# Kernel tuning notes

Measured on AMD Instinct MI355X. Metric: run time of the kernel, lower is better.

Reference implementation:

```python
import jax, jax.numpy as jnp
import numpy as np

BETA = 1.0
POWER_ITERS = 9
EPS = 1e-12  # F.normalize default eps


def _normalize(v):
    # L2 normalize over dim=1 of [B, N, 1], matching F.normalize(x, dim=1)
    n = jnp.linalg.norm(v, axis=1, keepdims=True)
    return v / jnp.maximum(n, EPS)


def _dominant_eigenvalue(A, x):
    # A: [B, N, N], x: [B, N, 1]
    for _ in range(POWER_ITERS):
        x = _normalize(jnp.matmul(A, x))
    Ax = jnp.matmul(A, x)[..., 0]              # [B, N]
    num = jnp.sum(Ax * x[..., 0], axis=1)      # x^T A x
    den = jnp.sum(x[..., 0] ** 2, axis=1)      # ||x||^2 (== 1 after normalize)
    return num / den, x


def setup_inputs() -> dict:
    key = jax.random.key(0)
    k1, k2 = jax.random.split(key)
    B, C, H, W = 256, 2048, 7, 7
    x = jax.random.normal(k1, (B, C, H, W), dtype=jnp.float32)
    x0 = _normalize(jax.random.normal(k2, (B, H * W, 1), dtype=jnp.float32))
    return {"x": x, "x0": x0}


def reference(x, x0):
    B, C, H, W = x.shape
    N = H * W
    Wm = x.reshape(B, C, N)
    # ATA = W^T W : [B, N, N]
    ATA = jnp.einsum('bcn,bcm->bnm', Wm, Wm)
    # first power iteration: largest eigenvalue; x0 is a no_grad constant
    largest, x1 = _dominant_eigenvalue(ATA, jax.lax.stop_gradient(x0))
    I = jnp.eye(N, dtype=ATA.dtype)
    shifted = ATA - largest[:, None, None] * I
    # second power iteration warm-started from detached x1 (torch stores last_x detached)
    tmp, _ = _dominant_eigenvalue(shifted, jax.lax.stop_gradient(x1))
    smallest = tmp + largest
    penalty = BETA * (largest / smallest - 1.0) ** 2
    return jnp.sum(penalty) / B
```

## Files before the change

### kernel.cpp

```cpp
#include <hip/hip_runtime.h>
#include <hip/hip_bf16.h>
#include <stdint.h>


#define BATCH 256
#define CDIM  2048
#define NDIM  49
#define GROUPS 2
#define GK    (CDIM / GROUPS)
#define CHUNK 64
#define NCHUNK (GK / CHUNK)
#define ITEMS (NDIM * (CHUNK / 8))
#define CHUNK_FLOATS (CHUNK * NDIM)

typedef __bf16 bf16x8 __attribute__((ext_vector_type(8)));
typedef float  f32x16 __attribute__((ext_vector_type(16)));
typedef float  f32x4  __attribute__((ext_vector_type(4)));

union V16 {
  f32x4  f4;
  bf16x8 b8;
};

__device__ __forceinline__ void load8(const float* __restrict__ g,
                                      float (&r)[8]) {
#pragma unroll
  for (int j = 0; j < 8; ++j) r[j] = g[j * NDIM];
}

__device__ __forceinline__ void cvt_store(const float (&r)[8], float* Hb,
                                          float* Lb, int w) {
  bf16x8 hv, lv;
#pragma unroll
  for (int j = 0; j < 8; ++j) {
    float e = r[j];
    __bf16 h = (__bf16)e;
    hv[j] = h;
    lv[j] = (__bf16)(e - (float)h);
  }
  V16 a, b;
  a.b8 = hv;
  b.b8 = lv;
  *(f32x4*)(Hb + w) = a.f4;
  *(f32x4*)(Lb + w) = b.f4;
}

__device__ __forceinline__ void comp16(const float* Hb, const float* Lb,
                                       int m, int n, int hf, f32x16& c1,
                                       f32x16& c2, f32x16& c3) {
  const f32x4* H = (const f32x4*)Hb;
  const f32x4* L = (const f32x4*)Lb;
#pragma unroll
  for (int s = 0; s < 4; ++s) {
    const int blk = 2 * s + hf;
    V16 ah, al, bh, bl;
    ah.f4 = H[m * 8 + (blk ^ (m & 7))];
    al.f4 = L[m * 8 + (blk ^ (m & 7))];
    bh.f4 = H[n * 8 + (blk ^ (n & 7))];
    bl.f4 = L[n * 8 + (blk ^ (n & 7))];
    c1 = __builtin_amdgcn_mfma_f32_32x32x16_bf16(ah.b8, bh.b8, c1, 0, 0, 0);
    c2 = __builtin_amdgcn_mfma_f32_32x32x16_bf16(ah.b8, bl.b8, c2, 0, 0, 0);
    c3 = __builtin_amdgcn_mfma_f32_32x32x16_bf16(al.b8, bh.b8, c3, 0, 0, 0);
  }
}

__global__ __launch_bounds__(512) void fused_kernel(
    const float* __restrict__ x, const float* __restrict__ x0,
    float* __restrict__ pen) {
  __shared__ __align__(16) float lds[GROUPS * 8192];
  __shared__ __align__(16) float A[NDIM * NDIM + 3];

  const int tid  = threadIdx.x;
  const int b    = blockIdx.x;
  const int g    = tid >> 8;
  const int ltid = tid & 255;
  const int lane = tid & 63;
  const int gw   = (tid >> 6) & 3;
  const int ln   = lane & 31;
  const int hf   = lane >> 5;
  const int qm = gw >> 1, qn = gw & 1;
  const int m = qm * 32 + ln;
  const int n = qn * 32 + ln;

  float* const buf0 = lds + g * 8192;
  float* const buf1 = lds + g * 8192 + 4096;

  const float* gbase = x + (size_t)b * (CDIM * NDIM)
                         + (size_t)g * (GK * NDIM);

  const int i0 = ltid;
  const int i1 = ltid + 256;
  const bool v1 = (i1 < ITEMS);
  const int kq0 = (i0 * 1338) >> 16;
  const int n0  = i0 - 49 * kq0;
  const int kq1 = (i1 * 1338) >> 16;
  const int n1  = i1 - 49 * kq1;
  const int g0  = kq0 * (8 * NDIM) + n0;
  const int g1  = kq1 * (8 * NDIM) + n1;
  const int w0  = n0 * 32 + 4 * (kq0 ^ (n0 & 7));
  const int w1  = n1 * 32 + 4 * (kq1 ^ (n1 & 7));

  f32x16 c1, c2, c3;
#pragma unroll
  for (int i = 0; i < 16; ++i) { c1[i] = 0.f; c2[i] = 0.f; c3[i] = 0.f; }

  float sA0[8], sA1[8], sB0[8], sB1[8];

  load8(gbase + g0, sA0);
  if (v1) load8(gbase + g1, sA1);

  for (int ch = 0; ch < NCHUNK; ch += 2) {
    {
      const float* gch = gbase + (size_t)(ch + 1) * CHUNK_FLOATS;
      load8(gch + g0, sB0);
      if (v1) load8(gch + g1, sB1);
    }
    cvt_store(sA0, buf0, buf0 + 2048, w0);
    if (v1) cvt_store(sA1, buf0, buf0 + 2048, w1);
    __syncthreads();
    comp16(buf0, buf0 + 2048, m, n, hf, c1, c2, c3);

    if (ch + 2 < NCHUNK) {
      const float* gch = gbase + (size_t)(ch + 2) * CHUNK_FLOATS;
      load8(gch + g0, sA0);
      if (v1) load8(gch + g1, sA1);
    }
    cvt_store(sB0, buf1, buf1 + 2048, w0);
    if (v1) cvt_store(sB1, buf1, buf1 + 2048, w1);
    __syncthreads();
    comp16(buf1, buf1 + 2048, m, n, hf, c1, c2, c3);
  }

  __syncthreads();
#pragma unroll
  for (int gg = 0; gg < GROUPS; ++gg) {
    if (g == gg) {
#pragma unroll
      for (int r = 0; r < 16; ++r) {
        int row = (r & 3) + 8 * (r >> 2) + 4 * hf;
        int mm = qm * 32 + row;
        if (mm < NDIM && n < NDIM) {
          float v = c1[r] + c2[r] + c3[r];
          if (gg == 0) A[mm * NDIM + n] = v;
          else         A[mm * NDIM + n] += v;
        }
      }
    }
    __syncthreads();
  }

  if (tid < 64) {
    const bool act = (tid < NDIM);
    float Ar[NDIM];
    {
      const float* Arow = &A[(act ? tid : (NDIM - 1)) * NDIM];
#pragma unroll
      for (int k = 0; k < NDIM; ++k) Ar[k] = Arow[k];
    }
    float xl = act ? x0[b * NDIM + tid] : 0.f;

    auto rayleigh = [&](float shift) -> float {
      for (int it = 0; it < 9; ++it) {
        float a0r = 0.f, a1r = 0.f, a2r = 0.f, a3r = 0.f;
#pragma unroll
        for (int k = 0; k < 48; k += 4) {
          a0r = fmaf(Ar[k + 0], __shfl(xl, k + 0, 64), a0r);
          a1r = fmaf(Ar[k + 1], __shfl(xl, k + 1, 64), a1r);
          a2r = fmaf(Ar[k + 2], __shfl(xl, k + 2, 64), a2r);
          a3r = fmaf(Ar[k + 3], __shfl(xl, k + 3, 64), a3r);
        }
        a0r = fmaf(Ar[48], __shfl(xl, 48, 64), a0r);
        float y = act ? (((a0r + a1r) + (a2r + a3r)) - shift * xl) : 0.f;
        float s2 = y * y;
#pragma unroll
        for (int o = 32; o; o >>= 1) s2 += __shfl_xor(s2, o, 64);
        xl = y / fmaxf(sqrtf(s2), 1e-12f);
      }
      float a0r = 0.f, a1r = 0.f, a2r = 0.f, a3r = 0.f;
#pragma unroll
      for (int k = 0; k < 48; k += 4) {
        a0r = fmaf(Ar[k + 0], __shfl(xl, k + 0, 64), a0r);
        a1r = fmaf(Ar[k + 1], __shfl(xl, k + 1, 64), a1r);
        a2r = fmaf(Ar[k + 2], __shfl(xl, k + 2, 64), a2r);
        a3r = fmaf(Ar[k + 3], __shfl(xl, k + 3, 64), a3r);
      }
      a0r = fmaf(Ar[48], __shfl(xl, 48, 64), a0r);
      float yy = act ? (((a0r + a1r) + (a2r + a3r)) - shift * xl) : 0.f;
      float num = yy * xl;
      float den = xl * xl;
#pragma unroll
      for (int o = 32; o; o >>= 1) {
        num += __shfl_xor(num, o, 64);
        den += __shfl_xor(den, o, 64);
      }
      return num / den;
    };

    float largest  = rayleigh(0.f);
    float smallest = rayleigh(largest) + largest;
    if (tid == 0) {
      float r = largest / smallest - 1.f;
      pen[b] = r * r;
    }
  }
}

__global__ __launch_bounds__(64) void finish_kernel(
    const float* __restrict__ pen, float* __restrict__ out) {
  const int t = threadIdx.x;
  float s = pen[t] + pen[t + 64] + pen[t + 128] + pen[t + 192];
#pragma unroll
  for (int o = 32; o; o >>= 1) s += __shfl_xor(s, o, 64);
  if (t == 0) out[0] = s * (1.0f / (float)BATCH);
}

extern "C" void kernel_launch(void* const* d_in, const int* in_sizes, int n_in,
                              void* d_out, int out_size, void* d_ws,
                              size_t ws_size, hipStream_t stream) {
  const float* x  = (const float*)d_in[0];
  const float* x0 = (const float*)d_in[1];
  float* out = (float*)d_out;
  float* pen = (float*)d_ws;

  fused_kernel<<<BATCH, 512, 0, stream>>>(x, x0, pen);
  finish_kernel<<<1, 64, 0, stream>>>(pen, out);
}
```

Before: 165.3 us.

## Split fused kernel into per-half Gram blocks and separate eigen kernel

Restructures the work so each batch's Gram matrix is computed by two independent 256-thread blocks (one per channel half), which write partial 49x49 results to workspace. A separate 64-thread-per-batch kernel sums the partials and runs the power iterations, and the final sum uses an atomicAdd instead of a finish kernel. The aim is more blocks for better CU occupancy and no serial eigen tail holding a 512-thread block's resources. In exchange it adds global round-trips for the partials and makes the summation order nondeterministic through atomics.

```diff
diff --git a/kernel.cpp b/kernel.cpp
--- a/kernel.cpp
+++ b/kernel.cpp
@@ -6,12 +6,13 @@
 #define BATCH 256
 #define CDIM  2048
 #define NDIM  49
-#define GROUPS 2
-#define GK    (CDIM / GROUPS)
+#define HALVES 2
+#define GK    (CDIM / HALVES)
 #define CHUNK 64
 #define NCHUNK (GK / CHUNK)
 #define ITEMS (NDIM * (CHUNK / 8))
 #define CHUNK_FLOATS (CHUNK * NDIM)
+#define PSTRIDE 2404
 
 typedef __bf16 bf16x8 __attribute__((ext_vector_type(8)));
 typedef float  f32x16 __attribute__((ext_vector_type(16)));
@@ -64,32 +65,33 @@
   }
 }
 
-__global__ __launch_bounds__(512) void fused_kernel(
-    const float* __restrict__ x, const float* __restrict__ x0,
-    float* __restrict__ pen) {
-  __shared__ __align__(16) float lds[GROUPS * 8192];
-  __shared__ __align__(16) float A[NDIM * NDIM + 3];
+__global__ __launch_bounds__(256, 2) void gram_kernel(
+    const float* __restrict__ x, float* __restrict__ partial,
+    float* __restrict__ out) {
+  __shared__ __align__(16) float lds[8192];
 
   const int tid  = threadIdx.x;
-  const int b    = blockIdx.x;
-  const int g    = tid >> 8;
-  const int ltid = tid & 255;
+  const int bidx = blockIdx.x;
+  const int batch = bidx >> 1;
+  const int half  = bidx & 1;
   const int lane = tid & 63;
-  const int gw   = (tid >> 6) & 3;
+  const int wv   = tid >> 6;
   const int ln   = lane & 31;
   const int hf   = lane >> 5;
-  const int qm = gw >> 1, qn = gw & 1;
+  const int qm = wv >> 1, qn = wv & 1;
   const int m = qm * 32 + ln;
   const int n = qn * 32 + ln;
 
-  float* const buf0 = lds + g * 8192;
-  float* const buf1 = lds + g * 8192 + 4096;
-
-  const float* gbase = x + (size_t)b * (CDIM * NDIM)
-                         + (size_t)g * (GK * NDIM);
-
-  const int i0 = ltid;
-  const int i1 = ltid + 256;
+  if (bidx == 0 && tid == 0) out[0] = 0.f;
+
+  float* const buf0 = lds;
+  float* const buf1 = lds + 4096;
+
+  const float* gbase = x + (size_t)batch * (CDIM * NDIM)
+                         + (size_t)half * (GK * NDIM);
+
+  const int i0 = tid;
+  const int i1 = tid + 256;
   const bool v1 = (i1 < ITEMS);
   const int kq0 = (i0 * 1338) >> 16;
   const int n0  = i0 - 49 * kq0;
@@ -131,51 +133,34 @@
     comp16(buf1, buf1 + 2048, m, n, hf, c1, c2, c3);
   }
 
-  __syncthreads();
-#pragma unroll
-  for (int gg = 0; gg < GROUPS; ++gg) {
-    if (g == gg) {
-#pragma unroll
-      for (int r = 0; r < 16; ++r) {
-        int row = (r & 3) + 8 * (r >> 2) + 4 * hf;
-        int mm = qm * 32 + row;
-        if (mm < NDIM && n < NDIM) {
-          float v = c1[r] + c2[r] + c3[r];
-          if (gg == 0) A[mm * NDIM + n] = v;
-          else         A[mm * NDIM + n] += v;
-        }
-      }
-    }
-    __syncthreads();
-  }
-
-  if (tid < 64) {
-    const bool act = (tid < NDIM);
-    float Ar[NDIM];
-    {
-      const float* Arow = &A[(act ? tid : (NDIM - 1)) * NDIM];
-#pragma unroll
-      for (int k = 0; k < NDIM; ++k) Ar[k] = Arow[k];
-    }
-    float xl = act ? x0[b * NDIM + tid] : 0.f;
-
-    auto rayleigh = [&](float shift) -> float {
-      for (int it = 0; it < 9; ++it) {
-        float a0r = 0.f, a1r = 0.f, a2r = 0.f, a3r = 0.f;
-#pragma unroll
-        for (int k = 0; k < 48; k += 4) {
-          a0r = fmaf(Ar[k + 0], __shfl(xl, k + 0, 64), a0r);
-          a1r = fmaf(Ar[k + 1], __shfl(xl, k + 1, 64), a1r);
-          a2r = fmaf(Ar[k + 2], __shfl(xl, k + 2, 64), a2r);
-          a3r = fmaf(Ar[k + 3], __shfl(xl, k + 3, 64), a3r);
-        }
-        a0r = fmaf(Ar[48], __shfl(xl, 48, 64), a0r);
-        float y = act ? (((a0r + a1r) + (a2r + a3r)) - shift * xl) : 0.f;
-        float s2 = y * y;
-#pragma unroll
-        for (int o = 32; o; o >>= 1) s2 += __shfl_xor(s2, o, 64);
-        xl = y / fmaxf(sqrtf(s2), 1e-12f);
-      }
+  float* outp = partial + (size_t)bidx * PSTRIDE;
+#pragma unroll
+  for (int r = 0; r < 16; ++r) {
+    int row = (r & 3) + 8 * (r >> 2) + 4 * hf;
+    int mm = qm * 32 + row;
+    if (mm < NDIM && n < NDIM)
+      outp[mm * NDIM + n] = c1[r] + c2[r] + c3[r];
+  }
+}
+
+__global__ __launch_bounds__(64) void eigen_kernel(
+    const float* __restrict__ partial, const float* __restrict__ x0,
+    float* __restrict__ out) {
+  const int b = blockIdx.x;
+  const int t = threadIdx.x;
+  const bool act = (t < NDIM);
+  const int row = act ? t : (NDIM - 1);
+
+  const float* rp0 = partial + (size_t)(2 * b) * PSTRIDE + row * NDIM;
+  const float* rp1 = partial + (size_t)(2 * b + 1) * PSTRIDE + row * NDIM;
+  float Ar[NDIM];
+#pragma unroll
+  for (int k = 0; k < NDIM; ++k) Ar[k] = rp0[k] + rp1[k];
+
+  float xl = act ? x0[b * NDIM + t] : 0.f;
+
+  auto rayleigh = [&](float shift) -> float {
+    for (int it = 0; it < 9; ++it) {
       float a0r = 0.f, a1r = 0.f, a2r = 0.f, a3r = 0.f;
 #pragma unroll
       for (int k = 0; k < 48; k += 4) {
@@ -185,33 +170,38 @@
         a3r = fmaf(Ar[k + 3], __shfl(xl, k + 3, 64), a3r);
       }
       a0r = fmaf(Ar[48], __shfl(xl, 48, 64), a0r);
-      float yy = act ? (((a0r + a1r) + (a2r + a3r)) - shift * xl) : 0.f;
-      float num = yy * xl;
-      float den = xl * xl;
-#pragma unroll
-      for (int o = 32; o; o >>= 1) {
-        num += __shfl_xor(num, o, 64);
-        den += __shfl_xor(den, o, 64);
-      }
-      return num / den;
-    };
-
-    float largest  = rayleigh(0.f);
-    float smallest = rayleigh(largest) + largest;
-    if (tid == 0) {
-      float r = largest / smallest - 1.f;
-      pen[b] = r * r;
-    }
-  }
-}
-
-__global__ __launch_bounds__(64) void finish_kernel(
-    const float* __restrict__ pen, float* __restrict__ out) {
-  const int t = threadIdx.x;
-  float s = pen[t] + pen[t + 64] + pen[t + 128] + pen[t + 192];
-#pragma unroll
-  for (int o = 32; o; o >>= 1) s += __shfl_xor(s, o, 64);
-  if (t == 0) out[0] = s * (1.0f / (float)BATCH);
+      float y = act ? (((a0r + a1r) + (a2r + a3r)) - shift * xl) : 0.f;
+      float s2 = y * y;
+#pragma unroll
+      for (int o = 32; o; o >>= 1) s2 += __shfl_xor(s2, o, 64);
+      xl = y / fmaxf(sqrtf(s2), 1e-12f);
+    }
+    float a0r = 0.f, a1r = 0.f, a2r = 0.f, a3r = 0.f;
+#pragma unroll
+    for (int k = 0; k < 48; k += 4) {
+      a0r = fmaf(Ar[k + 0], __shfl(xl, k + 0, 64), a0r);
+      a1r = fmaf(Ar[k + 1], __shfl(xl, k + 1, 64), a1r);
+      a2r = fmaf(Ar[k + 2], __shfl(xl, k + 2, 64), a2r);
+      a3r = fmaf(Ar[k + 3], __shfl(xl, k + 3, 64), a3r);
+    }
+    a0r = fmaf(Ar[48], __shfl(xl, 48, 64), a0r);
+    float yy = act ? (((a0r + a1r) + (a2r + a3r)) - shift * xl) : 0.f;
+    float num = yy * xl;
+    float den = xl * xl;
+#pragma unroll
+    for (int o = 32; o; o >>= 1) {
+      num += __shfl_xor(num, o, 64);
+      den += __shfl_xor(den, o, 64);
+    }
+    return num / den;
+  };
+
+  float largest  = rayleigh(0.f);
+  float smallest = rayleigh(largest) + largest;
+  if (t == 0) {
+    float r = largest / smallest - 1.f;
+    atomicAdd(out, r * r * (1.0f / (float)BATCH));
+  }
 }
 
 extern "C" void kernel_launch(void* const* d_in, const int* in_sizes, int n_in,
@@ -220,8 +210,8 @@
   const float* x  = (const float*)d_in[0];
   const float* x0 = (const float*)d_in[1];
   float* out = (float*)d_out;
-  float* pen = (float*)d_ws;
-
-  fused_kernel<<<BATCH, 512, 0, stream>>>(x, x0, pen);
-  finish_kernel<<<1, 64, 0, stream>>>(pen, out);
-}
+  float* partial = (float*)d_ws;
+
+  gram_kernel<<<512, 256, 0, stream>>>(x, partial, out);
+  eigen_kernel<<<BATCH, 64, 0, stream>>>(partial, x0, out);
+}
```

Result: no change. 167.7 us (+1.5%).
